# Kernel tuning notes

Hardware: AMD Instinct MI355X
Metric: run time of the kernel (lower is better)

The kernel has to match this reference:

```python
import jax, jax.numpy as jnp
import numpy as np

B, S, D_IN, D_OUT = 4, 2048, 1024, 1024


def setup_inputs() -> dict:
    key = jax.random.key(0)
    k1, k2, k3, k4 = jax.random.split(key, 4)
    scale = 1.0 / np.sqrt(D_IN)
    return {
        "x": jax.random.normal(k1, (B, S, D_IN), dtype=jnp.float32),
        "W_q": jax.random.normal(k2, (D_IN, D_OUT), dtype=jnp.float32) * scale,
        "W_k": jax.random.normal(k3, (D_IN, D_OUT), dtype=jnp.float32) * scale,
        "W_v": jax.random.normal(k4, (D_IN, D_OUT), dtype=jnp.float32) * scale,
    }


def reference(x, W_q, W_k, W_v):
    # x: [B, S, D_IN]; weights stored as [D_IN, D_OUT] (transpose of torch Linear)
    q = x @ W_q  # [B, S, D_OUT]
    k = x @ W_k
    v = x @ W_v
    inv_sqrt_d = 1.0 / jnp.sqrt(jnp.asarray(k.shape[-1], dtype=q.dtype))
    scores = jnp.einsum("bqd,bkd->bqk", q, k) * inv_sqrt_d  # [B, S, S]
    n = x.shape[1]
    causal_mask = jnp.triu(jnp.ones((n, n), dtype=bool), k=1)  # True above diagonal
    scores = jnp.where(causal_mask, -jnp.inf, scores)
    attn = jax.nn.softmax(scores, axis=-1)  # dropout p=0.0 -> identity
    return jnp.einsum("bqk,bkd->bqd", attn, v)  # [B, S, D_OUT]
```

## Files before the change

kernel.cpp:

```cpp
#include <hip/hip_runtime.h>
#include <hip/hip_bf16.h>
#include <stdint.h>

typedef __bf16 bf16;
typedef bf16 bf16x8 __attribute__((ext_vector_type(8)));
typedef float f32x4 __attribute__((ext_vector_type(4)));

#define NB   4
#define SS   2048
#define DI   1024
#define DOUT 1024

__device__ __forceinline__ void gload_lds16(const void* g, void* l) {
  __builtin_amdgcn_global_load_lds(
      (const __attribute__((address_space(1))) void*)g,
      (__attribute__((address_space(3))) void*)l, 16, 0, 0);
}

#define BARX  { __builtin_amdgcn_s_barrier(); __builtin_amdgcn_sched_barrier(0); }
#define VMW12 asm volatile("s_waitcnt vmcnt(12)" ::: "memory")
#define VMW8  asm volatile("s_waitcnt vmcnt(8)"  ::: "memory")
#define VMW6  asm volatile("s_waitcnt vmcnt(6)"  ::: "memory")
#define VMW4  asm volatile("s_waitcnt vmcnt(4)"  ::: "memory")
#define VMW0  asm volatile("s_waitcnt vmcnt(0)"  ::: "memory")

__device__ __forceinline__ bf16x8 cvt8(float4 a, float4 b) {
  bf16x8 v;
  v[0] = (bf16)a.x; v[1] = (bf16)a.y; v[2] = (bf16)a.z; v[3] = (bf16)a.w;
  v[4] = (bf16)b.x; v[5] = (bf16)b.y; v[6] = (bf16)b.z; v[7] = (bf16)b.w;
  return v;
}

__device__ __forceinline__ void r5_loop3(
    const bf16* __restrict__ Ag, int lda,
    const bf16* __restrict__ Bg, int ldb,
    int nt, char* lds, f32x4 (&acc)[8][4])
{
  const int tid = threadIdx.x, lane = tid & 63, w = tid >> 6;
  const int g    = (tid & 3) ^ ((tid >> 3) & 3);
  const int srow = tid >> 2;
  const int l15  = lane & 15, lg = lane >> 4;
  const int aoff = l15 * 64 + ((lg ^ ((l15 >> 1) & 3)) << 4);

  auto STG = [&](int t, int p) {
    char* Ab = lds + p * 24576;
    char* Bb = lds + p * 24576 + 8192;
#pragma unroll
    for (int i = 0; i < 2; ++i)
      gload_lds16(Ag + (size_t)(i * 64 + srow) * lda + t * 32 + g * 8,
                  Ab + i * 4096 + tid * 16);
#pragma unroll
    for (int i = 0; i < 4; ++i)
      gload_lds16(Bg + (size_t)(i * 64 + srow) * ldb + t * 32 + g * 8,
                  Bb + i * 4096 + tid * 16);
  };

  auto CMP = [&](int p) {
    const char* Ab = lds + p * 24576;
    const char* Bb = lds + p * 24576 + 8192 + w * 4096;
    bf16x8 a[8], bq[4];
#pragma unroll
    for (int am = 0; am < 8; ++am) a[am] = *(const bf16x8*)(Ab + am * 1024 + aoff);
#pragma unroll
    for (int fn = 0; fn < 4; ++fn) bq[fn] = *(const bf16x8*)(Bb + fn * 1024 + aoff);
    __builtin_amdgcn_s_setprio(1);
#pragma unroll
    for (int am = 0; am < 8; ++am)
#pragma unroll
      for (int fn = 0; fn < 4; ++fn)
        acc[am][fn] = __builtin_amdgcn_mfma_f32_16x16x32_bf16(
            a[am], bq[fn], acc[am][fn], 0, 0, 0);
    __builtin_amdgcn_s_setprio(0);
  };

  STG(0, 0);
  STG(1, 1);
  int pw = 2, pr = 0;
  for (int t = 0; t < nt - 2; ++t) {
    STG(t + 2, pw);
    VMW12;
    BARX;
    CMP(pr);
    BARX;
    pw = (pw == 2) ? 0 : pw + 1;
    pr = (pr == 2) ? 0 : pr + 1;
  }
  VMW6; BARX; CMP(pr); BARX;
  pr = (pr == 2) ? 0 : pr + 1;
  VMW0; BARX; CMP(pr);
}

__device__ __forceinline__ void r5h_loop3(
    const bf16* __restrict__ Ag, int lda,
    const bf16* __restrict__ Bg, int ldb,
    int nt, char* lds, f32x4 (&acc)[4][4])
{
  const int tid = threadIdx.x, lane = tid & 63, wid = tid >> 6;
  const int wr = wid >> 1, wc = wid & 1;
  const int g    = (tid & 3) ^ ((tid >> 3) & 3);
  const int srow = tid >> 2;
  const int l15  = lane & 15, lg = lane >> 4;
  const int aoff = l15 * 64 + ((lg ^ ((l15 >> 1) & 3)) << 4);

  auto STG = [&](int t, int p) {
    char* Ab = lds + p * 16384;
    char* Bb = lds + p * 16384 + 8192;
#pragma unroll
    for (int i = 0; i < 2; ++i) {
      gload_lds16(Ag + (size_t)(i * 64 + srow) * lda + t * 32 + g * 8,
                  Ab + i * 4096 + tid * 16);
      gload_lds16(Bg + (size_t)(i * 64 + srow) * ldb + t * 32 + g * 8,
                  Bb + i * 4096 + tid * 16);
    }
  };

  auto CMP = [&](int p) {
    const char* Ab = lds + p * 16384 + wr * 4096;
    const char* Bb = lds + p * 16384 + 8192 + wc * 4096;
    bf16x8 a[4], bq[4];
#pragma unroll
    for (int fm = 0; fm < 4; ++fm) a[fm] = *(const bf16x8*)(Ab + fm * 1024 + aoff);
#pragma unroll
    for (int fn = 0; fn < 4; ++fn) bq[fn] = *(const bf16x8*)(Bb + fn * 1024 + aoff);
    __builtin_amdgcn_s_setprio(1);
#pragma unroll
    for (int fm = 0; fm < 4; ++fm)
#pragma unroll
      for (int fn = 0; fn < 4; ++fn)
        acc[fm][fn] = __builtin_amdgcn_mfma_f32_16x16x32_bf16(
            a[fm], bq[fn], acc[fm][fn], 0, 0, 0);
    __builtin_amdgcn_s_setprio(0);
  };

  STG(0, 0);
  STG(1, 1);
  int pw = 2, pr = 0;
  for (int t = 0; t < nt - 2; ++t) {
    STG(t + 2, pw);
    VMW8;
    BARX;
    CMP(pr);
    BARX;
    pw = (pw == 2) ? 0 : pw + 1;
    pr = (pr == 2) ? 0 : pr + 1;
  }
  VMW4; BARX; CMP(pr); BARX;
  pr = (pr == 2) ? 0 : pr + 1;
  VMW0; BARX; CMP(pr);
}

__device__ __forceinline__ void acc_zero4(f32x4 (&acc)[4][4]) {
#pragma unroll
  for (int i = 0; i < 4; ++i)
#pragma unroll
    for (int j = 0; j < 4; ++j)
      acc[i][j] = (f32x4){0.f, 0.f, 0.f, 0.f};
}

__global__ __launch_bounds__(256) void k_castx_mtp(const float* __restrict__ x,
                                                   bf16* __restrict__ xb,
                                                   const float* __restrict__ Wq,
                                                   const float* __restrict__ Wk,
                                                   const float* __restrict__ Wv,
                                                   bf16* __restrict__ WTv,
                                                   float* __restrict__ MTp) {
  __shared__ __align__(16) char lds[16384];
  const int bid = blockIdx.x;
  const int tid = threadIdx.x;

  if (bid < 512) {
    const int tile = bid >> 3, s = bid & 7;
    const int m0 = (tile >> 3) * 128, n0 = (tile & 7) * 128;
    const int k0 = s * 128;
    const int lane = tid & 63, wid = tid >> 6;
    const int wr = wid >> 1, wc = wid & 1;
    const int g    = (tid & 3) ^ ((tid >> 3) & 3);
    const int srow = tid >> 2;
    const int l15  = lane & 15, lg = lane >> 4;
    const int aoff = l15 * 64 + ((lg ^ ((l15 >> 1) & 3)) << 4);

    f32x4 acc[4][4];
    acc_zero4(acc);

    for (int t = 0; t < 4; ++t) {
#pragma unroll
      for (int i = 0; i < 2; ++i) {
        const float* ap = Wk + (size_t)(m0 + i * 64 + srow) * DI + k0 + t * 32 + g * 8;
        const float* bp = Wq + (size_t)(n0 + i * 64 + srow) * DI + k0 + t * 32 + g * 8;
        const float4 a0 = *(const float4*)ap, a1 = *(const float4*)(ap + 4);
        const float4 b0 = *(const float4*)bp, b1 = *(const float4*)(bp + 4);
        *(bf16x8*)(lds + i * 4096 + tid * 16)        = cvt8(a0, a1);
        *(bf16x8*)(lds + 8192 + i * 4096 + tid * 16) = cvt8(b0, b1);
      }
      __syncthreads();
      {
        const char* Ab = lds + wr * 4096;
        const char* Bb = lds + 8192 + wc * 4096;
        bf16x8 a[4], bq[4];
#pragma unroll
        for (int fm = 0; fm < 4; ++fm) a[fm] = *(const bf16x8*)(Ab + fm * 1024 + aoff);
#pragma unroll
        for (int fn = 0; fn < 4; ++fn) bq[fn] = *(const bf16x8*)(Bb + fn * 1024 + aoff);
#pragma unroll
        for (int fm = 0; fm < 4; ++fm)
#pragma unroll
          for (int fn = 0; fn < 4; ++fn)
            acc[fm][fn] = __builtin_amdgcn_mfma_f32_16x16x32_bf16(
                a[fm], bq[fn], acc[fm][fn], 0, 0, 0);
      }
      __syncthreads();
    }

    float* MPs = MTp + (size_t)s * 1024 * 1024;
    const int r4 = (lane >> 4) * 4, cn = lane & 15;
#pragma unroll
    for (int fm = 0; fm < 4; ++fm)
#pragma unroll
      for (int fn = 0; fn < 4; ++fn) {
        const int rowb = m0 + wr * 64 + fm * 16 + r4;
        const int col  = n0 + wc * 64 + fn * 16 + cn;
#pragma unroll
        for (int rr = 0; rr < 4; ++rr)
          MPs[(size_t)(rowb + rr) * 1024 + col] = acc[fm][fn][rr];
      }
  } else if (bid < 4608) {
    const size_t i = ((size_t)(bid - 512) * 256 + tid) * 8;
    const float4 a = *(const float4*)(x + i);
    const float4 c = *(const float4*)(x + i + 4);
    *(bf16x8*)(xb + i) = cvt8(a, c);
  } else {
    float (*t)[33] = (float (*)[33])lds;
    const int tt = bid - 4608;
    const int c0 = (tt & 31) * 32, k0 = (tt >> 5) * 32;
    const int tx = tid & 31, ty = tid >> 5;
#pragma unroll
    for (int i = 0; i < 4; ++i)
      t[ty + 8 * i][tx] = Wv[(size_t)(k0 + ty + 8 * i) * DI + c0 + tx];
    __syncthreads();
#pragma unroll
    for (int i = 0; i < 4; ++i)
      WTv[(size_t)(c0 + ty + 8 * i) * DI + k0 + tx] = (bf16)t[tx][ty + 8 * i];
  }
}

__global__ __launch_bounds__(256) void k_mtred(const float* __restrict__ MTp,
                                               bf16* __restrict__ MT) {
  const size_t i = ((size_t)blockIdx.x * 256 + threadIdx.x) * 8;
  float4 a = *(const float4*)(MTp + i);
  float4 b = *(const float4*)(MTp + i + 4);
#pragma unroll
  for (int s = 1; s < 8; ++s) {
    const float* p = MTp + (size_t)s * 1024 * 1024 + i;
    const float4 c = *(const float4*)p;
    const float4 d = *(const float4*)(p + 4);
    a.x += c.x; a.y += c.y; a.z += c.z; a.w += c.w;
    b.x += d.x; b.y += d.y; b.z += d.z; b.w += d.w;
  }
  *(bf16x8*)(MT + i) = cvt8(a, b);
}

__global__ __launch_bounds__(256, 2) void k_tv(const bf16* __restrict__ X,
                                               const bf16* __restrict__ MT,
                                               const bf16* __restrict__ WTv,
                                               bf16* __restrict__ T,
                                               bf16* __restrict__ VT) {
  __shared__ __align__(16) char lds[73728];
  const int bid  = blockIdx.x;
  const int wgid = (bid & 7) * 64 + (bid >> 3);
  const int m0 = (wgid >> 3) * 128;
  const int n0 = (wgid & 7) * 256;

  const bf16* Bg = (n0 < 1024) ? MT + (size_t)n0 * 1024
                               : WTv + (size_t)(n0 - 1024) * 1024;

  f32x4 acc[8][4];
#pragma unroll
  for (int i = 0; i < 8; ++i)
#pragma unroll
    for (int j = 0; j < 4; ++j)
      acc[i][j] = (f32x4){0.f, 0.f, 0.f, 0.f};

  r5_loop3(X + (size_t)m0 * 1024, 1024, Bg, 1024, 32, lds, acc);

  const int lane = threadIdx.x & 63, w = threadIdx.x >> 6;
  const int r4 = (lane >> 4) * 4;
  const int cn = lane & 15;
  if (n0 < 1024) {
#pragma unroll
    for (int am = 0; am < 8; ++am) {
      const int row = m0 + am * 16 + r4;
#pragma unroll
      for (int fn = 0; fn < 4; ++fn) {
        const int n = n0 + w * 64 + fn * 16 + cn;
        const size_t base = (size_t)row * 1024 + n;
#pragma unroll
        for (int r = 0; r < 4; ++r)
          T[base + (size_t)r * 1024] = (bf16)acc[am][fn][r];
      }
    }
  } else {
    const int b_ = m0 >> 11;
    const int sb = m0 & 2047;
#pragma unroll
    for (int am = 0; am < 8; ++am)
#pragma unroll
      for (int fn = 0; fn < 4; ++fn) {
        const int d  = (n0 - 1024) + w * 64 + fn * 16 + cn;
        const int s0 = sb + am * 16 + r4;
        ushort4 pk;
        pk.x = __builtin_bit_cast(unsigned short, (bf16)acc[am][fn][0]);
        pk.y = __builtin_bit_cast(unsigned short, (bf16)acc[am][fn][1]);
        pk.z = __builtin_bit_cast(unsigned short, (bf16)acc[am][fn][2]);
        pk.w = __builtin_bit_cast(unsigned short, (bf16)acc[am][fn][3]);
        *(ushort4*)(VT + ((size_t)b_ * DOUT + d) * SS + s0) = pk;
      }
  }
}

__global__ __launch_bounds__(256, 3) void k_gemm_qk(const bf16* __restrict__ T,
                                                    const bf16* __restrict__ XB,
                                                    bf16* __restrict__ E,
                                                    float* __restrict__ RS) {
  __shared__ __align__(16) char lds[49152];
  const int wfl = blockIdx.x;
  const int b = wfl / 136;
  int r = wfl % 136;
  int i = 0;
  for (;;) { const int cnt = i + 1; if (r < cnt) break; r -= cnt; ++i; }
  const int m0 = i * 128, n0 = r * 128;

  f32x4 acc[4][4];
  acc_zero4(acc);
  r5h_loop3(T  + ((size_t)b * SS + m0) * 1024, 1024,
            XB + ((size_t)b * SS + n0) * 1024, 1024, 32, lds, acc);

  bf16* Eb = E + (size_t)b * SS * SS;
  float* RSb = RS + (size_t)b * SS;
  const float scale = 0.03125f;
  const int lane = threadIdx.x & 63, wid = threadIdx.x >> 6;
  const int wr = wid >> 1, wc = wid & 1;
  const int r4 = (lane >> 4) * 4, cn = lane & 15;

  float rsum[4][4];
#pragma unroll
  for (int fm = 0; fm < 4; ++fm)
#pragma unroll
    for (int rr = 0; rr < 4; ++rr) rsum[fm][rr] = 0.f;

#pragma unroll
  for (int fm = 0; fm < 4; ++fm)
#pragma unroll
    for (int fn = 0; fn < 4; ++fn) {
      const int n = n0 + wc * 64 + fn * 16 + cn;
      const int rowb = m0 + wr * 64 + fm * 16 + r4;
      const size_t bofs = (size_t)rowb * SS + n;
#pragma unroll
      for (int rr = 0; rr < 4; ++rr) {
        const float e = (n <= rowb + rr) ? __expf(acc[fm][fn][rr] * scale) : 0.f;
        Eb[bofs + (size_t)rr * SS] = (bf16)e;
        rsum[fm][rr] += e;
      }
    }

#pragma unroll
  for (int fm = 0; fm < 4; ++fm)
#pragma unroll
    for (int rr = 0; rr < 4; ++rr) {
      float s = rsum[fm][rr];
      s += __shfl_xor(s, 1);
      s += __shfl_xor(s, 2);
      s += __shfl_xor(s, 4);
      s += __shfl_xor(s, 8);
      if (cn == 0)
        atomicAdd(&RSb[m0 + wr * 64 + fm * 16 + r4 + rr], s);
    }
}

__global__ __launch_bounds__(256, 3) void k_gemm_pv(const bf16* __restrict__ P,
                                                    const bf16* __restrict__ VT,
                                                    const float* __restrict__ RS,
                                                    float* __restrict__ Out) {
  __shared__ __align__(16) char lds[49152];
  const int wfl = blockIdx.x;
  const int h = wfl >> 8;
  const int r = wfl & 255;
  const int b = r >> 6;
  const int t = r & 63;
  const int ip = t >> 3;
  const int j = t & 7;
  const int i = h ? (15 - ip) : ip;
  const int m0 = i * 128, n0 = j * 128;
  const int nt = 4 * (i + 1);

  f32x4 acc[4][4];
  acc_zero4(acc);
  r5h_loop3(P  + (size_t)b * SS * SS   + (size_t)m0 * SS, SS,
            VT + (size_t)b * DOUT * SS + (size_t)n0 * SS, SS,
            nt, lds, acc);

  float* Ob = Out + (size_t)b * SS * DOUT;
  const float* RSb = RS + (size_t)b * SS;
  const int lane = threadIdx.x & 63, wid = threadIdx.x >> 6;
  const int wr = wid >> 1, wc = wid & 1;
  const int r4 = (lane >> 4) * 4, cn = lane & 15;
#pragma unroll
  for (int fm = 0; fm < 4; ++fm) {
    const int rowb = m0 + wr * 64 + fm * 16 + r4;
    const float4 rs4 = *(const float4*)(RSb + rowb);
    float inv[4];
    inv[0] = 1.0f / rs4.x; inv[1] = 1.0f / rs4.y;
    inv[2] = 1.0f / rs4.z; inv[3] = 1.0f / rs4.w;
#pragma unroll
    for (int fn = 0; fn < 4; ++fn) {
      const int n = n0 + wc * 64 + fn * 16 + cn;
      const size_t bofs = (size_t)rowb * DOUT + n;
#pragma unroll
      for (int rr = 0; rr < 4; ++rr)
        Ob[bofs + (size_t)rr * DOUT] = acc[fm][fn][rr] * inv[rr];
    }
  }
}

extern "C" void kernel_launch(void* const* d_in, const int* in_sizes, int n_in,
                              void* d_out, int out_size, void* d_ws, size_t ws_size,
                              hipStream_t stream) {
  const float* x  = (const float*)d_in[0];
  const float* Wq = (const float*)d_in[1];
  const float* Wk = (const float*)d_in[2];
  const float* Wv = (const float*)d_in[3];
  float* out = (float*)d_out;
  char* ws = (char*)d_ws;

  bf16*  T   = (bf16*)(ws);
  bf16*  VT  = (bf16*)(ws + ((size_t)16 << 20));
  bf16*  E   = (bf16*)(ws + ((size_t)32 << 20));
  float* MTp = (float*)(ws + ((size_t)32 << 20));
  bf16*  XB  = (bf16*)(ws + ((size_t)64 << 20));
  bf16*  WTv = (bf16*)(ws + ((size_t)80 << 20));
  bf16*  MT  = (bf16*)(ws + ((size_t)82 << 20));
  float* RS  = (float*)(ws + ((size_t)84 << 20));

  hipMemsetAsync(RS, 0, (size_t)NB * SS * sizeof(float), stream);
  k_castx_mtp<<<5632, 256, 0, stream>>>(x, XB, Wq, Wk, Wv, WTv, MTp);
  k_mtred<<<512, 256, 0, stream>>>(MTp, MT);
  k_tv<<<512, 256, 0, stream>>>(XB, MT, WTv, T, VT);
  k_gemm_qk<<<544, 256, 0, stream>>>(T, XB, E, RS);
  k_gemm_pv<<<512, 256, 0, stream>>>(E, VT, RS, out);
}
```

Baseline: 147.5 us.

## Fuse split-K partial reduction into prep kernel via atomic tile counters

Cuts the W_k·W_q^T split-K factor from 8 to 4 slices, each covering 256 of K. The last block to finish each output tile, detected with an atomic counter, reduces the partials and writes the bf16 result. This removes the separate k_mtred launch and halves the partial-buffer traffic. In exchange there are fewer, longer GEMM blocks, a serialized tail reduction in the last block of each tile, and extra memset for the counters.

Result: slower. 200.7 us (+36.1%).

```diff
diff --git a/kernel.cpp b/kernel.cpp
--- a/kernel.cpp
+++ b/kernel.cpp
@@ -157,21 +157,24 @@
       acc[i][j] = (f32x4){0.f, 0.f, 0.f, 0.f};
 }
 
-__global__ __launch_bounds__(256) void k_castx_mtp(const float* __restrict__ x,
-                                                   bf16* __restrict__ xb,
-                                                   const float* __restrict__ Wq,
-                                                   const float* __restrict__ Wk,
-                                                   const float* __restrict__ Wv,
-                                                   bf16* __restrict__ WTv,
-                                                   float* __restrict__ MTp) {
+__global__ __launch_bounds__(256) void k_prep(const float* __restrict__ x,
+                                              bf16* __restrict__ xb,
+                                              const float* __restrict__ Wq,
+                                              const float* __restrict__ Wk,
+                                              const float* __restrict__ Wv,
+                                              bf16* __restrict__ WTv,
+                                              float* __restrict__ MTp,
+                                              bf16* __restrict__ MT,
+                                              int* __restrict__ CNT) {
   __shared__ __align__(16) char lds[16384];
+  __shared__ int s_old;
   const int bid = blockIdx.x;
   const int tid = threadIdx.x;
 
-  if (bid < 512) {
-    const int tile = bid >> 3, s = bid & 7;
+  if (bid < 256) {
+    const int tile = bid >> 2, s = bid & 3;
     const int m0 = (tile >> 3) * 128, n0 = (tile & 7) * 128;
-    const int k0 = s * 128;
+    const int k0 = s * 256;
     const int lane = tid & 63, wid = tid >> 6;
     const int wr = wid >> 1, wc = wid & 1;
     const int g    = (tid & 3) ^ ((tid >> 3) & 3);
@@ -182,7 +185,7 @@
     f32x4 acc[4][4];
     acc_zero4(acc);
 
-    for (int t = 0; t < 4; ++t) {
+    for (int t = 0; t < 8; ++t) {
 #pragma unroll
       for (int i = 0; i < 2; ++i) {
         const float* ap = Wk + (size_t)(m0 + i * 64 + srow) * DI + k0 + t * 32 + g * 8;
@@ -211,7 +214,7 @@
       __syncthreads();
     }
 
-    float* MPs = MTp + (size_t)s * 1024 * 1024;
+    float* MPs = MTp + (size_t)s * (1024 * 1024);
     const int r4 = (lane >> 4) * 4, cn = lane & 15;
 #pragma unroll
     for (int fm = 0; fm < 4; ++fm)
@@ -223,14 +226,38 @@
         for (int rr = 0; rr < 4; ++rr)
           MPs[(size_t)(rowb + rr) * 1024 + col] = acc[fm][fn][rr];
       }
-  } else if (bid < 4608) {
-    const size_t i = ((size_t)(bid - 512) * 256 + tid) * 8;
+
+    __threadfence();
+    __syncthreads();
+    if (tid == 0) s_old = atomicAdd(&CNT[tile], 1);
+    __syncthreads();
+    if (s_old == 3) {
+      __threadfence();
+      const int r = m0 + (tid >> 1);
+      const int cb = n0 + (tid & 1) * 64;
+#pragma unroll
+      for (int c = 0; c < 8; ++c) {
+        const size_t off = (size_t)r * 1024 + cb + c * 8;
+        float4 a = {0.f, 0.f, 0.f, 0.f}, b = {0.f, 0.f, 0.f, 0.f};
+#pragma unroll
+        for (int s2 = 0; s2 < 4; ++s2) {
+          const float* p = MTp + (size_t)s2 * (1024 * 1024) + off;
+          const float4 u = *(const float4*)p;
+          const float4 v = *(const float4*)(p + 4);
+          a.x += u.x; a.y += u.y; a.z += u.z; a.w += u.w;
+          b.x += v.x; b.y += v.y; b.z += v.z; b.w += v.w;
+        }
+        *(bf16x8*)(MT + off) = cvt8(a, b);
+      }
+    }
+  } else if (bid < 4352) {
+    const size_t i = ((size_t)(bid - 256) * 256 + tid) * 8;
     const float4 a = *(const float4*)(x + i);
     const float4 c = *(const float4*)(x + i + 4);
     *(bf16x8*)(xb + i) = cvt8(a, c);
   } else {
     float (*t)[33] = (float (*)[33])lds;
-    const int tt = bid - 4608;
+    const int tt = bid - 4352;
     const int c0 = (tt & 31) * 32, k0 = (tt >> 5) * 32;
     const int tx = tid & 31, ty = tid >> 5;
 #pragma unroll
@@ -241,22 +268,6 @@
     for (int i = 0; i < 4; ++i)
       WTv[(size_t)(c0 + ty + 8 * i) * DI + k0 + tx] = (bf16)t[tx][ty + 8 * i];
   }
-}
-
-__global__ __launch_bounds__(256) void k_mtred(const float* __restrict__ MTp,
-                                               bf16* __restrict__ MT) {
-  const size_t i = ((size_t)blockIdx.x * 256 + threadIdx.x) * 8;
-  float4 a = *(const float4*)(MTp + i);
-  float4 b = *(const float4*)(MTp + i + 4);
-#pragma unroll
-  for (int s = 1; s < 8; ++s) {
-    const float* p = MTp + (size_t)s * 1024 * 1024 + i;
-    const float4 c = *(const float4*)p;
-    const float4 d = *(const float4*)(p + 4);
-    a.x += c.x; a.y += c.y; a.z += c.z; a.w += c.w;
-    b.x += d.x; b.y += d.y; b.z += d.z; b.w += d.w;
-  }
-  *(bf16x8*)(MT + i) = cvt8(a, b);
 }
 
 __global__ __launch_bounds__(256, 2) void k_tv(const bf16* __restrict__ X,
@@ -439,10 +450,10 @@
   bf16*  WTv = (bf16*)(ws + ((size_t)80 << 20));
   bf16*  MT  = (bf16*)(ws + ((size_t)82 << 20));
   float* RS  = (float*)(ws + ((size_t)84 << 20));
-
-  hipMemsetAsync(RS, 0, (size_t)NB * SS * sizeof(float), stream);
-  k_castx_mtp<<<5632, 256, 0, stream>>>(x, XB, Wq, Wk, Wv, WTv, MTp);
-  k_mtred<<<512, 256, 0, stream>>>(MTp, MT);
+  int*   CNT = (int*)(ws + ((size_t)84 << 20) + 32768);
+
+  hipMemsetAsync(RS, 0, 32768 + 256, stream);
+  k_prep<<<5376, 256, 0, stream>>>(x, XB, Wq, Wk, Wv, WTv, MTp, MT, CNT);
   k_tv<<<512, 256, 0, stream>>>(XB, MT, WTv, T, VT);
   k_gemm_qk<<<544, 256, 0, stream>>>(T, XB, E, RS);
   k_gemm_pv<<<512, 256, 0, stream>>>(E, VT, RS, out);
```
